# Optimization experiments

Measured on AMD Instinct MI355X. Metric: run time of the kernel, lower is better.

Reference implementation:

```python
import jax, jax.numpy as jnp
import numpy as np

BLOCK_SIZE = 2048
HEAD_SIZE = 64
N_EMBD = 768


def setup_inputs() -> dict:
    key = jax.random.key(0)
    k1, k2, k3 = jax.random.split(key, 3)
    x = jax.random.normal(k1, (8, 2048, N_EMBD), dtype=jnp.float32)
    Wq = jax.random.normal(k2, (N_EMBD, HEAD_SIZE), dtype=jnp.float32) * (N_EMBD ** -0.5)
    rel_table = jax.random.normal(k3, (2 * BLOCK_SIZE - 1, 1), dtype=jnp.float32)
    return {"x": x, "Wq": Wq, "rel_table": rel_table}


def reference(x, Wq, rel_table):
    B, T, C = x.shape
    # NOTE: original module uses self.query for q, k AND v (faithful reproduction)
    q = x @ Wq  # [B, T, H]
    k = q
    v = q
    max_rel = BLOCK_SIZE - 1
    pos = jnp.arange(T)
    rel = pos[None, :] - pos[:, None]            # [T, T]
    rel_idx = jnp.clip(rel, -max_rel, max_rel) + max_rel
    bias = rel_table[rel_idx, 0][None, :, :]     # [1, T, T]
    scores = jnp.einsum('bth,bsh->bts', q, k) * (HEAD_SIZE ** -0.5)
    scores = scores + bias
    causal = pos[None, :] <= pos[:, None]        # [T, T] lower-triangular
    scores = jnp.where(causal[None, :, :], scores, -jnp.inf)
    attn = jax.nn.softmax(scores, axis=-1)       # dropout p=0.0 -> identity
    out = jnp.einsum('bts,bsh->bth', attn, v)    # [B, T, H]
    return out
```

## Files before the change

### kernel.cpp

```cpp
#include <hip/hip_runtime.h>
#include <hip/hip_fp16.h>

typedef _Float16 half8 __attribute__((ext_vector_type(8)));
typedef _Float16 half4 __attribute__((ext_vector_type(4)));
typedef float floatx4 __attribute__((ext_vector_type(4)));

#define T_SEQ 2048
#define NB    8

#define GLOBAL_AS __attribute__((address_space(1)))
#define LDS_AS    __attribute__((address_space(3)))

__global__ __launch_bounds__(256) void prep_kernel(
    const float* __restrict__ Wq, const float* __restrict__ rel,
    _Float16* __restrict__ WqT, float* __restrict__ biasS)
{
  const int bid = blockIdx.x, tid = threadIdx.x;
  if (bid < 64) {
    for (int k = tid; k < 768; k += 256)
      WqT[bid * 768 + k] = (_Float16)Wq[k * 64 + bid];
  } else {
    for (int i = tid; i < 4095; i += 256)
      biasS[i] = rel[i] * 1.44269504f;
  }
}

__global__ __launch_bounds__(256, 2) void qproj_kernel(
    const float* __restrict__ x, const _Float16* __restrict__ WqT,
    const float* __restrict__ rel,
    _Float16* __restrict__ q16, _Float16* __restrict__ q16T,
    float* __restrict__ Ct)
{
  __shared__ __align__(16) float xbuf[16 * 772];
  __shared__ float part[2 * 16 * 66];
  __shared__ float sumsq[16];
  _Float16* qs = (_Float16*)xbuf;

  const int tid  = threadIdx.x;
  const int w    = tid >> 6, lane = tid & 63;
  const int n    = lane & 15, quad = lane >> 4;
  const int k0   = w * 192;

  const _Float16* wp = WqT + (size_t)n * 768 + k0 + quad * 8;
  half8 Breg[6][4];
  #pragma unroll
  for (int i = 0; i < 6; ++i)
    #pragma unroll
    for (int t = 0; t < 4; ++t)
      Breg[i][t] = *(const half8*)(wp + 32 * i + t * 16 * 768);

  const float b0v = rel[2047] * 1.44269504f;
  float* partw = part + (w & 1) * 1056;

  #pragma unroll 1
  for (int it = 0; it < 2; ++it) {
    const int r0 = (blockIdx.x + it * 512) * 16;

    __syncthreads();

    #pragma unroll
    for (int r = 0; r < 4; ++r) {
      #pragma unroll
      for (int c = 0; c < 3; ++c) {
        const float* gp = x + (size_t)(r0 + 4 * w + r) * 768 + c * 256 + lane * 4;
        float* lp = xbuf + (4 * w + r) * 772 + c * 256 + lane * 4;
        __builtin_amdgcn_global_load_lds((const GLOBAL_AS void*)gp,
                                         (LDS_AS void*)lp, 16, 0, 0);
      }
    }
    __builtin_amdgcn_s_waitcnt(0x0f70);
    __syncthreads();

    floatx4 acc[4];
    #pragma unroll
    for (int s = 0; s < 4; ++s) acc[s] = (floatx4){0.f, 0.f, 0.f, 0.f};

    #pragma unroll
    for (int i = 0; i < 6; ++i) {
      const float* ap = xbuf + n * 772 + k0 + 32 * i + quad * 8;
      float4 x0 = *(const float4*)ap;
      float4 x1 = *(const float4*)(ap + 4);
      half8 a;
      a[0] = (_Float16)x0.x; a[1] = (_Float16)x0.y;
      a[2] = (_Float16)x0.z; a[3] = (_Float16)x0.w;
      a[4] = (_Float16)x1.x; a[5] = (_Float16)x1.y;
      a[6] = (_Float16)x1.z; a[7] = (_Float16)x1.w;
      acc[0] = __builtin_amdgcn_mfma_f32_16x16x32_f16(a, Breg[i][0], acc[0], 0, 0, 0);
      acc[1] = __builtin_amdgcn_mfma_f32_16x16x32_f16(a, Breg[i][1], acc[1], 0, 0, 0);
      acc[2] = __builtin_amdgcn_mfma_f32_16x16x32_f16(a, Breg[i][2], acc[2], 0, 0, 0);
      acc[3] = __builtin_amdgcn_mfma_f32_16x16x32_f16(a, Breg[i][3], acc[3], 0, 0, 0);
    }

    if (w < 2) {
      #pragma unroll
      for (int sub = 0; sub < 4; ++sub)
        #pragma unroll
        for (int r = 0; r < 4; ++r)
          partw[(4 * quad + r) * 66 + sub * 16 + n] = acc[sub][r];
    }
    __syncthreads();
    if (w >= 2) {
      #pragma unroll
      for (int sub = 0; sub < 4; ++sub)
        #pragma unroll
        for (int r = 0; r < 4; ++r)
          partw[(4 * quad + r) * 66 + sub * 16 + n] += acc[sub][r];
    }
    __syncthreads();

    #pragma unroll
    for (int k = 0; k < 4; ++k) {
      int e = tid + k * 256;
      int row = e >> 6, h = e & 63;
      float s = part[row * 66 + h] + part[1056 + row * 66 + h];
      q16[(size_t)(r0 + row) * 64 + h] = (_Float16)s;
      qs[row * 66 + h] = (_Float16)s;
      float ss = s * s;
      #pragma unroll
      for (int off = 1; off < 64; off <<= 1) ss += __shfl_xor(ss, off);
      if (lane == 0) sumsq[row] = ss;
    }
    __syncthreads();

    if (tid < 16)
      Ct[r0 + tid] = sumsq[tid] * 0.18033688f + b0v + 8.0f;

    {
      const int h = tid >> 2, rq = (tid & 3) * 4;
      half4 hv;
      hv[0] = qs[(rq + 0) * 66 + h]; hv[1] = qs[(rq + 1) * 66 + h];
      hv[2] = qs[(rq + 2) * 66 + h]; hv[3] = qs[(rq + 3) * 66 + h];
      const int bb = r0 >> 11, tt = r0 & 2047;
      *(half4*)(q16T + (size_t)(bb * 64 + h) * T_SEQ + tt + rq) = hv;
    }
  }
}

__global__ __launch_bounds__(256, 2) void attn_kernel(
    const _Float16* __restrict__ q16, const _Float16* __restrict__ q16T,
    const float* __restrict__ biasS, const float* __restrict__ Ct,
    float* __restrict__ out)
{
  __shared__ __align__(16) _Float16 Pbuf[4 * 16 * 72];
  __shared__ float Obuf[4 * 16 * 65];
  __shared__ float Lbuf[4 * 16];
  __shared__ float biasL[2080];

  const int bi = blockIdx.x;
  const int b  = bi & 7;
  const int p  = bi >> 3;

  const int tid  = threadIdx.x;
  const int w    = tid >> 6;
  const int lane = tid & 63;
  const int n    = lane & 15, quad = lane >> 4;

  _Float16* Pw = Pbuf + w * 1152;
  const float ksc = 0.125f * 1.44269504f;
  const _Float16* vbase = q16T + (size_t)(b * 64 + n) * T_SEQ + quad * 8;
  const half8 ones = {(_Float16)1, (_Float16)1, (_Float16)1, (_Float16)1,
                      (_Float16)1, (_Float16)1, (_Float16)1, (_Float16)1};

  #define LOAD_KV(S0, K, V)                                                   \
    {                                                                         \
      _Pragma("unroll")                                                       \
      for (int sub = 0; sub < 4; ++sub) {                                     \
        const _Float16* kp =                                                  \
            q16 + (size_t)(b * T_SEQ + (S0) + sub * 16 + n) * 64 + quad * 8;  \
        K[2 * sub]     = *(const half8*)kp;                                   \
        K[2 * sub + 1] = *(const half8*)(kp + 32);                            \
      }                                                                       \
      _Pragma("unroll")                                                       \
      for (int sh = 0; sh < 4; ++sh) {                                        \
        V[sh]     = *(const half8*)(vbase + (size_t)(sh * 16) * T_SEQ + (S0));\
        V[4 + sh] = *(const half8*)(vbase + (size_t)(sh * 16) * T_SEQ + (S0) + 32); \
      }                                                                       \
    }

  #pragma unroll 1
  for (int ht = 0; ht < 2; ++ht) {
    const int qi = ht ? (127 - p) : p;
    const int t0 = qi * 16;
    const int kfull = t0 >> 6;

    {
      const int lo = 2032 - t0, cnt = t0 + 31;
      for (int i = tid; i < cnt; i += 256) biasL[i] = biasS[lo + i];
    }

    half8 aq0, aq1;
    {
      const _Float16* qrow = q16 + (size_t)(b * T_SEQ + t0 + n) * 64 + quad * 8;
      aq0 = *(const half8*)qrow;
      aq1 = *(const half8*)(qrow + 32);
    }
    float ctv[4];
    #pragma unroll
    for (int r = 0; r < 4; ++r)
      ctv[r] = Ct[b * T_SEQ + t0 + 4 * quad + r];

    floatx4 O[4];
    #pragma unroll
    for (int s = 0; s < 4; ++s) O[s] = (floatx4){0.f, 0.f, 0.f, 0.f};
    floatx4 den = (floatx4){0.f, 0.f, 0.f, 0.f};

    __syncthreads();

    half8 cK[8], cV[8], nK[8], nV[8];
    int kt = w;
    if (kt <= kfull) LOAD_KV(kt * 64, cK, cV);

    for (; kt <= kfull; kt += 4) {
      const int ktn = kt + 4;
      if (ktn <= kfull) LOAD_KV(ktn * 64, nK, nV);

      const int  s0 = kt * 64;
      const bool dg = (kt == kfull);
      const int  j  = (t0 - s0) >> 4;

      #pragma unroll
      for (int sub = 0; sub < 4; ++sub) {
        if (dg && sub > j) {
          #pragma unroll
          for (int r = 0; r < 4; ++r)
            Pw[(4 * quad + r) * 72 + sub * 16 + n] = (_Float16)0.f;
          continue;
        }
        floatx4 sc = (floatx4){0.f, 0.f, 0.f, 0.f};
        sc = __builtin_amdgcn_mfma_f32_16x16x32_f16(aq0, cK[2 * sub], sc, 0, 0, 0);
        sc = __builtin_amdgcn_mfma_f32_16x16x32_f16(aq1, cK[2 * sub + 1], sc, 0, 0, 0);
        const int smin = s0 + sub * 16;
        #pragma unroll
        for (int r = 0; r < 4; ++r) {
          float bv = biasL[15 + smin + n - 4 * quad - r];
          float pv = exp2f(fmaf(sc[r], ksc, bv) - ctv[r]);
          if (dg && sub == j && n > 4 * quad + r) pv = 0.f;
          Pw[(4 * quad + r) * 72 + sub * 16 + n] = (_Float16)pv;
        }
      }

      #pragma unroll
      for (int ch = 0; ch < 2; ++ch) {
        half8 pf = *(const half8*)(Pw + n * 72 + ch * 32 + quad * 8);
        den = __builtin_amdgcn_mfma_f32_16x16x32_f16(pf, ones, den, 0, 0, 0);
        #pragma unroll
        for (int sh = 0; sh < 4; ++sh)
          O[sh] = __builtin_amdgcn_mfma_f32_16x16x32_f16(pf, cV[ch * 4 + sh],
                                                         O[sh], 0, 0, 0);
      }

      #pragma unroll
      for (int i = 0; i < 8; ++i) { cK[i] = nK[i]; cV[i] = nV[i]; }
    }

    #pragma unroll
    for (int sub = 0; sub < 4; ++sub)
      #pragma unroll
      for (int r = 0; r < 4; ++r)
        Obuf[w * 1040 + (4 * quad + r) * 65 + sub * 16 + n] = O[sub][r];
    if (n == 0) {
      #pragma unroll
      for (int r = 0; r < 4; ++r)
        Lbuf[w * 16 + 4 * quad + r] = den[r];
    }
    __syncthreads();

    #pragma unroll
    for (int k = 0; k < 4; ++k) {
      const int e = tid + k * 256;
      const int row = e >> 6, h = e & 63;
      float num = Obuf[row * 65 + h]        + Obuf[1040 + row * 65 + h] +
                  Obuf[2080 + row * 65 + h] + Obuf[3120 + row * 65 + h];
      float d   = Lbuf[row] + Lbuf[16 + row] + Lbuf[32 + row] + Lbuf[48 + row];
      out[(size_t)(b * T_SEQ + t0 + row) * 64 + h] = num / d;
    }
  }
  #undef LOAD_KV
}

extern "C" void kernel_launch(void* const* d_in, const int* in_sizes, int n_in,
                              void* d_out, int out_size, void* d_ws, size_t ws_size,
                              hipStream_t stream) {
  const float* x   = (const float*)d_in[0];
  const float* Wq  = (const float*)d_in[1];
  const float* rel = (const float*)d_in[2];
  float* out = (float*)d_out;

  _Float16* q16   = (_Float16*)d_ws;
  _Float16* q16T  = q16  + (size_t)NB * T_SEQ * 64;
  _Float16* WqT   = q16T + (size_t)NB * T_SEQ * 64;
  float*    biasS = (float*)(WqT + 64 * 768);
  float*    Ct    = biasS + 4096;

  prep_kernel <<<65,  256, 0, stream>>>(Wq, rel, WqT, biasS);
  qproj_kernel<<<512, 256, 0, stream>>>(x, WqT, rel, q16, q16T, Ct);
  attn_kernel <<<512, 256, 0, stream>>>(q16, q16T, biasS, Ct, out);
}
```

Baseline: 134.9 us.

## Restructure qproj to single-wave blocks and widen attention to eight waves

The projection kernel now runs one 64-thread wave per 16-row tile. It streams x directly from global memory into registers with double buffering and reads Wq fragments on the fly, which removes the LDS staging, cross-wave partial-sum reduction and barriers. The attention kernel doubles to 8 waves per block so each wave handles fewer key tiles. It drops register prefetch of the next K/V tile and folds the bias scaling inline, which removes the separate biasS precompute. The trade-off is more global Wq reads and no software pipelining of K/V loads in attention, in exchange for more parallelism and less synchronization.

```diff
diff --git a/kernel.cpp b/kernel.cpp
--- a/kernel.cpp
+++ b/kernel.cpp
@@ -8,142 +8,102 @@
 #define T_SEQ 2048
 #define NB    8
 
-#define GLOBAL_AS __attribute__((address_space(1)))
-#define LDS_AS    __attribute__((address_space(3)))
-
 __global__ __launch_bounds__(256) void prep_kernel(
-    const float* __restrict__ Wq, const float* __restrict__ rel,
-    _Float16* __restrict__ WqT, float* __restrict__ biasS)
+    const float* __restrict__ Wq, _Float16* __restrict__ WqT)
 {
-  const int bid = blockIdx.x, tid = threadIdx.x;
-  if (bid < 64) {
-    for (int k = tid; k < 768; k += 256)
-      WqT[bid * 768 + k] = (_Float16)Wq[k * 64 + bid];
-  } else {
-    for (int i = tid; i < 4095; i += 256)
-      biasS[i] = rel[i] * 1.44269504f;
-  }
-}
-
-__global__ __launch_bounds__(256, 2) void qproj_kernel(
+  const int h = blockIdx.x, tid = threadIdx.x;
+  for (int k = tid; k < 768; k += 256)
+    WqT[h * 768 + k] = (_Float16)Wq[k * 64 + h];
+}
+
+__global__ __launch_bounds__(64, 2) void qproj_kernel(
     const float* __restrict__ x, const _Float16* __restrict__ WqT,
     const float* __restrict__ rel,
     _Float16* __restrict__ q16, _Float16* __restrict__ q16T,
     float* __restrict__ Ct)
 {
-  __shared__ __align__(16) float xbuf[16 * 772];
-  __shared__ float part[2 * 16 * 66];
-  __shared__ float sumsq[16];
-  _Float16* qs = (_Float16*)xbuf;
-
-  const int tid  = threadIdx.x;
-  const int w    = tid >> 6, lane = tid & 63;
-  const int n    = lane & 15, quad = lane >> 4;
-  const int k0   = w * 192;
-
-  const _Float16* wp = WqT + (size_t)n * 768 + k0 + quad * 8;
-  half8 Breg[6][4];
-  #pragma unroll
-  for (int i = 0; i < 6; ++i)
-    #pragma unroll
-    for (int t = 0; t < 4; ++t)
-      Breg[i][t] = *(const half8*)(wp + 32 * i + t * 16 * 768);
+  const int lane = threadIdx.x;
+  const int n = lane & 15, quad = lane >> 4;
+  const int r0 = blockIdx.x * 16;
+
+  const float*    xp = x   + (size_t)(r0 + n) * 768 + quad * 8;
+  const _Float16* wp = WqT + (size_t)n * 768 + quad * 8;
+
+  float4 A[2][8];
+  #pragma unroll
+  for (int i = 0; i < 4; ++i) {
+    A[0][2 * i]     = *(const float4*)(xp + 32 * i);
+    A[0][2 * i + 1] = *(const float4*)(xp + 32 * i + 4);
+  }
+
+  floatx4 acc[4];
+  #pragma unroll
+  for (int s = 0; s < 4; ++s) acc[s] = (floatx4){0.f, 0.f, 0.f, 0.f};
+
+  #pragma unroll
+  for (int g = 0; g < 6; ++g) {
+    const int cur = g & 1, nxt = cur ^ 1;
+    if (g < 5) {
+      #pragma unroll
+      for (int i = 0; i < 4; ++i) {
+        A[nxt][2 * i]     = *(const float4*)(xp + 128 * (g + 1) + 32 * i);
+        A[nxt][2 * i + 1] = *(const float4*)(xp + 128 * (g + 1) + 32 * i + 4);
+      }
+    }
+    #pragma unroll
+    for (int i = 0; i < 4; ++i) {
+      const int kc = 128 * g + 32 * i;
+      half8 b0 = *(const half8*)(wp + kc);
+      half8 b1 = *(const half8*)(wp + 16 * 768 + kc);
+      half8 b2 = *(const half8*)(wp + 32 * 768 + kc);
+      half8 b3 = *(const half8*)(wp + 48 * 768 + kc);
+      half8 a;
+      a[0] = (_Float16)A[cur][2 * i].x; a[1] = (_Float16)A[cur][2 * i].y;
+      a[2] = (_Float16)A[cur][2 * i].z; a[3] = (_Float16)A[cur][2 * i].w;
+      a[4] = (_Float16)A[cur][2 * i + 1].x; a[5] = (_Float16)A[cur][2 * i + 1].y;
+      a[6] = (_Float16)A[cur][2 * i + 1].z; a[7] = (_Float16)A[cur][2 * i + 1].w;
+      acc[0] = __builtin_amdgcn_mfma_f32_16x16x32_f16(a, b0, acc[0], 0, 0, 0);
+      acc[1] = __builtin_amdgcn_mfma_f32_16x16x32_f16(a, b1, acc[1], 0, 0, 0);
+      acc[2] = __builtin_amdgcn_mfma_f32_16x16x32_f16(a, b2, acc[2], 0, 0, 0);
+      acc[3] = __builtin_amdgcn_mfma_f32_16x16x32_f16(a, b3, acc[3], 0, 0, 0);
+    }
+  }
 
   const float b0v = rel[2047] * 1.44269504f;
-  float* partw = part + (w & 1) * 1056;
-
-  #pragma unroll 1
-  for (int it = 0; it < 2; ++it) {
-    const int r0 = (blockIdx.x + it * 512) * 16;
-
-    __syncthreads();
-
+  float ss[4] = {0.f, 0.f, 0.f, 0.f};
+  const int bb = r0 >> 11, tt = (r0 & 2047) + quad * 4;
+  #pragma unroll
+  for (int sub = 0; sub < 4; ++sub) {
+    half4 hv;
     #pragma unroll
     for (int r = 0; r < 4; ++r) {
-      #pragma unroll
-      for (int c = 0; c < 3; ++c) {
-        const float* gp = x + (size_t)(r0 + 4 * w + r) * 768 + c * 256 + lane * 4;
-        float* lp = xbuf + (4 * w + r) * 772 + c * 256 + lane * 4;
-        __builtin_amdgcn_global_load_lds((const GLOBAL_AS void*)gp,
-                                         (LDS_AS void*)lp, 16, 0, 0);
-      }
-    }
-    __builtin_amdgcn_s_waitcnt(0x0f70);
-    __syncthreads();
-
-    floatx4 acc[4];
-    #pragma unroll
-    for (int s = 0; s < 4; ++s) acc[s] = (floatx4){0.f, 0.f, 0.f, 0.f};
-
-    #pragma unroll
-    for (int i = 0; i < 6; ++i) {
-      const float* ap = xbuf + n * 772 + k0 + 32 * i + quad * 8;
-      float4 x0 = *(const float4*)ap;
-      float4 x1 = *(const float4*)(ap + 4);
-      half8 a;
-      a[0] = (_Float16)x0.x; a[1] = (_Float16)x0.y;
-      a[2] = (_Float16)x0.z; a[3] = (_Float16)x0.w;
-      a[4] = (_Float16)x1.x; a[5] = (_Float16)x1.y;
-      a[6] = (_Float16)x1.z; a[7] = (_Float16)x1.w;
-      acc[0] = __builtin_amdgcn_mfma_f32_16x16x32_f16(a, Breg[i][0], acc[0], 0, 0, 0);
-      acc[1] = __builtin_amdgcn_mfma_f32_16x16x32_f16(a, Breg[i][1], acc[1], 0, 0, 0);
-      acc[2] = __builtin_amdgcn_mfma_f32_16x16x32_f16(a, Breg[i][2], acc[2], 0, 0, 0);
-      acc[3] = __builtin_amdgcn_mfma_f32_16x16x32_f16(a, Breg[i][3], acc[3], 0, 0, 0);
-    }
-
-    if (w < 2) {
-      #pragma unroll
-      for (int sub = 0; sub < 4; ++sub)
-        #pragma unroll
-        for (int r = 0; r < 4; ++r)
-          partw[(4 * quad + r) * 66 + sub * 16 + n] = acc[sub][r];
-    }
-    __syncthreads();
-    if (w >= 2) {
-      #pragma unroll
-      for (int sub = 0; sub < 4; ++sub)
-        #pragma unroll
-        for (int r = 0; r < 4; ++r)
-          partw[(4 * quad + r) * 66 + sub * 16 + n] += acc[sub][r];
-    }
-    __syncthreads();
-
-    #pragma unroll
-    for (int k = 0; k < 4; ++k) {
-      int e = tid + k * 256;
-      int row = e >> 6, h = e & 63;
-      float s = part[row * 66 + h] + part[1056 + row * 66 + h];
-      q16[(size_t)(r0 + row) * 64 + h] = (_Float16)s;
-      qs[row * 66 + h] = (_Float16)s;
-      float ss = s * s;
-      #pragma unroll
-      for (int off = 1; off < 64; off <<= 1) ss += __shfl_xor(ss, off);
-      if (lane == 0) sumsq[row] = ss;
-    }
-    __syncthreads();
-
-    if (tid < 16)
-      Ct[r0 + tid] = sumsq[tid] * 0.18033688f + b0v + 8.0f;
-
-    {
-      const int h = tid >> 2, rq = (tid & 3) * 4;
-      half4 hv;
-      hv[0] = qs[(rq + 0) * 66 + h]; hv[1] = qs[(rq + 1) * 66 + h];
-      hv[2] = qs[(rq + 2) * 66 + h]; hv[3] = qs[(rq + 3) * 66 + h];
-      const int bb = r0 >> 11, tt = r0 & 2047;
-      *(half4*)(q16T + (size_t)(bb * 64 + h) * T_SEQ + tt + rq) = hv;
-    }
-  }
-}
-
-__global__ __launch_bounds__(256, 2) void attn_kernel(
+      float v = acc[sub][r];
+      q16[(size_t)(r0 + quad * 4 + r) * 64 + sub * 16 + n] = (_Float16)v;
+      hv[r] = (_Float16)v;
+      ss[r] += v * v;
+    }
+    *(half4*)(q16T + (size_t)(bb * 64 + sub * 16 + n) * T_SEQ + tt) = hv;
+  }
+  #pragma unroll
+  for (int off = 1; off < 16; off <<= 1) {
+    #pragma unroll
+    for (int r = 0; r < 4; ++r) ss[r] += __shfl_xor(ss[r], off);
+  }
+  if (n == 0) {
+    #pragma unroll
+    for (int r = 0; r < 4; ++r)
+      Ct[r0 + quad * 4 + r] = ss[r] * 0.18033688f + b0v + 8.0f;
+  }
+}
+
+__global__ __launch_bounds__(512, 4) void attn_kernel(
     const _Float16* __restrict__ q16, const _Float16* __restrict__ q16T,
-    const float* __restrict__ biasS, const float* __restrict__ Ct,
+    const float* __restrict__ rel, const float* __restrict__ Ct,
     float* __restrict__ out)
 {
-  __shared__ __align__(16) _Float16 Pbuf[4 * 16 * 72];
-  __shared__ float Obuf[4 * 16 * 65];
-  __shared__ float Lbuf[4 * 16];
+  __shared__ __align__(16) _Float16 Pbuf[8 * 16 * 72];
+  __shared__ float Obuf[8 * 16 * 65];
+  __shared__ float Lbuf[8 * 16];
   __shared__ float biasL[2080];
 
   const int bi = blockIdx.x;
@@ -161,31 +121,17 @@
   const half8 ones = {(_Float16)1, (_Float16)1, (_Float16)1, (_Float16)1,
                       (_Float16)1, (_Float16)1, (_Float16)1, (_Float16)1};
 
-  #define LOAD_KV(S0, K, V)                                                   \
-    {                                                                         \
-      _Pragma("unroll")                                                       \
-      for (int sub = 0; sub < 4; ++sub) {                                     \
-        const _Float16* kp =                                                  \
-            q16 + (size_t)(b * T_SEQ + (S0) + sub * 16 + n) * 64 + quad * 8;  \
-        K[2 * sub]     = *(const half8*)kp;                                   \
-        K[2 * sub + 1] = *(const half8*)(kp + 32);                            \
-      }                                                                       \
-      _Pragma("unroll")                                                       \
-      for (int sh = 0; sh < 4; ++sh) {                                        \
-        V[sh]     = *(const half8*)(vbase + (size_t)(sh * 16) * T_SEQ + (S0));\
-        V[4 + sh] = *(const half8*)(vbase + (size_t)(sh * 16) * T_SEQ + (S0) + 32); \
-      }                                                                       \
-    }
-
   #pragma unroll 1
   for (int ht = 0; ht < 2; ++ht) {
     const int qi = ht ? (127 - p) : p;
     const int t0 = qi * 16;
     const int kfull = t0 >> 6;
 
+    __syncthreads();
+
     {
       const int lo = 2032 - t0, cnt = t0 + 31;
-      for (int i = tid; i < cnt; i += 256) biasL[i] = biasS[lo + i];
+      for (int i = tid; i < cnt; i += 512) biasL[i] = rel[lo + i] * 1.44269504f;
     }
 
     half8 aq0, aq1;
@@ -206,17 +152,24 @@
 
     __syncthreads();
 
-    half8 cK[8], cV[8], nK[8], nV[8];
-    int kt = w;
-    if (kt <= kfull) LOAD_KV(kt * 64, cK, cV);
-
-    for (; kt <= kfull; kt += 4) {
-      const int ktn = kt + 4;
-      if (ktn <= kfull) LOAD_KV(ktn * 64, nK, nV);
-
+    for (int kt = w; kt <= kfull; kt += 8) {
       const int  s0 = kt * 64;
       const bool dg = (kt == kfull);
       const int  j  = (t0 - s0) >> 4;
+
+      half8 cK[8], cV[8];
+      #pragma unroll
+      for (int sub = 0; sub < 4; ++sub) {
+        const _Float16* kp =
+            q16 + (size_t)(b * T_SEQ + s0 + sub * 16 + n) * 64 + quad * 8;
+        cK[2 * sub]     = *(const half8*)kp;
+        cK[2 * sub + 1] = *(const half8*)(kp + 32);
+      }
+      #pragma unroll
+      for (int sh = 0; sh < 4; ++sh) {
+        cV[sh]     = *(const half8*)(vbase + (size_t)(sh * 16) * T_SEQ + s0);
+        cV[4 + sh] = *(const half8*)(vbase + (size_t)(sh * 16) * T_SEQ + s0 + 32);
+      }
 
       #pragma unroll
       for (int sub = 0; sub < 4; ++sub) {
@@ -248,9 +201,6 @@
           O[sh] = __builtin_amdgcn_mfma_f32_16x16x32_f16(pf, cV[ch * 4 + sh],
                                                          O[sh], 0, 0, 0);
       }
-
-      #pragma unroll
-      for (int i = 0; i < 8; ++i) { cK[i] = nK[i]; cV[i] = nV[i]; }
     }
 
     #pragma unroll
@@ -266,16 +216,18 @@
     __syncthreads();
 
     #pragma unroll
-    for (int k = 0; k < 4; ++k) {
-      const int e = tid + k * 256;
+    for (int k = 0; k < 2; ++k) {
+      const int e = tid + k * 512;
       const int row = e >> 6, h = e & 63;
-      float num = Obuf[row * 65 + h]        + Obuf[1040 + row * 65 + h] +
-                  Obuf[2080 + row * 65 + h] + Obuf[3120 + row * 65 + h];
-      float d   = Lbuf[row] + Lbuf[16 + row] + Lbuf[32 + row] + Lbuf[48 + row];
+      float num = 0.f, d = 0.f;
+      #pragma unroll
+      for (int w8 = 0; w8 < 8; ++w8) {
+        num += Obuf[w8 * 1040 + row * 65 + h];
+        d   += Lbuf[w8 * 16 + row];
+      }
       out[(size_t)(b * T_SEQ + t0 + row) * 64 + h] = num / d;
     }
   }
-  #undef LOAD_KV
 }
 
 extern "C" void kernel_launch(void* const* d_in, const int* in_sizes, int n_in,
@@ -286,13 +238,12 @@
   const float* rel = (const float*)d_in[2];
   float* out = (float*)d_out;
 
-  _Float16* q16   = (_Float16*)d_ws;
-  _Float16* q16T  = q16  + (size_t)NB * T_SEQ * 64;
-  _Float16* WqT   = q16T + (size_t)NB * T_SEQ * 64;
-  float*    biasS = (float*)(WqT + 64 * 768);
-  float*    Ct    = biasS + 4096;
-
-  prep_kernel <<<65,  256, 0, stream>>>(Wq, rel, WqT, biasS);
-  qproj_kernel<<<512, 256, 0, stream>>>(x, WqT, rel, q16, q16T, Ct);
-  attn_kernel <<<512, 256, 0, stream>>>(q16, q16T, biasS, Ct, out);
-}
+  _Float16* q16  = (_Float16*)d_ws;
+  _Float16* q16T = q16  + (size_t)NB * T_SEQ * 64;
+  _Float16* WqT  = q16T + (size_t)NB * T_SEQ * 64;
+  float*    Ct   = (float*)(WqT + 64 * 768);
+
+  prep_kernel <<<64,   256, 0, stream>>>(Wq, WqT);
+  qproj_kernel<<<1024,  64, 0, stream>>>(x, WqT, rel, q16, q16T, Ct);
+  attn_kernel <<<512,  512, 0, stream>>>(q16, q16T, rel, Ct, out);
+}
```

After: 143.8 us. 6.6% more time.
